# Kernel optimization log

Measured on AMD Instinct MI355X. Metric: run time of the kernel, lower is better.

The kernel has to match this reference:

```python
import jax, jax.numpy as jnp
import numpy as np

B, N, DIM = 2, 2048, 1024
HEADS, DIM_HEAD = 16, 64
INNER = HEADS * DIM_HEAD  # 1024
SCALE = DIM_HEAD ** -0.5


def setup_inputs() -> dict:
    key = jax.random.key(0)
    ks = jax.random.split(key, 8)
    s = DIM ** -0.5
    return {
        "x1": jax.random.normal(ks[0], (B, N, DIM), jnp.float32),
        "x2": jax.random.normal(ks[1], (B, N, DIM), jnp.float32),
        "W_qkv1": jax.random.normal(ks[2], (DIM, INNER * 3), jnp.float32) * s,
        "W_qkv2": jax.random.normal(ks[3], (DIM, INNER * 3), jnp.float32) * s,
        "W_out1": jax.random.normal(ks[4], (INNER, DIM), jnp.float32) * s,
        "b_out1": jnp.zeros((DIM,), jnp.float32),
        "W_out2": jax.random.normal(ks[5], (INNER, DIM), jnp.float32) * s,
        "b_out2": jnp.zeros((DIM,), jnp.float32),
    }


def _split_heads(t):
    # [b, n, (h d)] -> [b, h, n, d]
    b, n, _ = t.shape
    return t.reshape(b, n, HEADS, DIM_HEAD).transpose(0, 2, 1, 3)


def _merge_heads(t):
    # [b, h, n, d] -> [b, n, (h d)]
    b, h, n, d = t.shape
    return t.transpose(0, 2, 1, 3).reshape(b, n, h * d)


def reference(x1, x2, W_qkv1, W_qkv2, W_out1, b_out1, W_out2, b_out2):
    qkv1 = x1 @ W_qkv1  # [b, n, 3*inner]
    qkv2 = x2 @ W_qkv2
    q1, k1, v1 = [_split_heads(t) for t in jnp.split(qkv1, 3, axis=-1)]
    q2, k2, v2 = [_split_heads(t) for t in jnp.split(qkv2, 3, axis=-1)]

    # direction 1: queries from stream 2 attend to keys/values of stream 1
    dots1 = jnp.einsum('bhid,bhjd->bhij', q2, k1) * SCALE
    attn1 = jax.nn.softmax(dots1, axis=-1)
    out1 = jnp.einsum('bhij,bhjd->bhid', attn1, v1)
    out1 = _merge_heads(out1) @ W_out1 + b_out1

    # direction 2: queries from stream 1 attend to keys/values of stream 2
    dots2 = jnp.einsum('bhid,bhjd->bhij', q1, k2) * SCALE
    attn2 = jax.nn.softmax(dots2, axis=-1)
    out2 = jnp.einsum('bhij,bhjd->bhid', attn2, v2)
    out2 = _merge_heads(out2) @ W_out2 + b_out2

    return (out1, out2)
```

## Files before the change

### kernel.cpp

```cpp
#include <hip/hip_runtime.h>
#include <cmath>

typedef __attribute__((ext_vector_type(8))) short short8;
typedef __attribute__((ext_vector_type(4))) float f32x4;
typedef __attribute__((ext_vector_type(16))) float f32x16;
using u16 = unsigned short;

#define DEV static __device__ __forceinline__

DEV u16 f2bf(float f) {
  union { float f; unsigned u; } v; v.f = f;
  unsigned r = v.u + 0x7FFFu + ((v.u >> 16) & 1u);
  return (u16)(r >> 16);
}

DEV unsigned cvtpk(float lo, float hi_) {
  unsigned d;
  asm("v_cvt_pk_bf16_f32 %0, %1, %2" : "=v"(d) : "v"(lo), "v"(hi_));
  return d;
}

DEV void gld16(const void* g, void* l) {
  __builtin_amdgcn_global_load_lds(
      (const __attribute__((address_space(1))) unsigned*)g,
      (__attribute__((address_space(3))) unsigned*)l, 16, 0, 0);
}

__global__ void probe_scale(float* out) {
  if (threadIdx.x == 0 && blockIdx.x == 0) {
    float b = __builtin_amdgcn_exp2f(1.0f);
    out[0] = 0.125f / logf(b);
    out[1] = (fabsf(b - 2.0f) < 1e-3f) ? 0.0f : 1.0f;
  }
}

__global__ __launch_bounds__(256) void conv_f32_bf16(const float* __restrict__ s0,
                                                     const float* __restrict__ s1,
                                                     u16* __restrict__ d0,
                                                     u16* __restrict__ d1, int n8) {
  const float* src = blockIdx.z ? s1 : s0;
  u16* dst = blockIdx.z ? d1 : d0;
  int i = blockIdx.x * 256 + threadIdx.x;
  if (i >= n8) return;
  const float4* s = reinterpret_cast<const float4*>(src) + (size_t)i * 2;
  float4 a = s[0], b = s[1];
  union { u16 s[8]; uint4 v; } t;
  t.s[0]=f2bf(a.x); t.s[1]=f2bf(a.y); t.s[2]=f2bf(a.z); t.s[3]=f2bf(a.w);
  t.s[4]=f2bf(b.x); t.s[5]=f2bf(b.y); t.s[6]=f2bf(b.z); t.s[7]=f2bf(b.w);
  reinterpret_cast<uint4*>(dst)[i] = t.v;
}

__global__ __launch_bounds__(256) void transpose_w(const float* __restrict__ s0,
                                                   const float* __restrict__ s1,
                                                   u16* __restrict__ d0,
                                                   u16* __restrict__ d1, int R, int C,
                                                   int qcols,
                                                   const float* __restrict__ qscale_p) {
  const float* src = blockIdx.z ? s1 : s0;
  u16* dst = blockIdx.z ? d1 : d0;
  const float qscale = qscale_p ? qscale_p[0] : 1.0f;
  __shared__ float tile[32][33];
  int tx = threadIdx.x & 31, ty = threadIdx.x >> 5;
  int rb = blockIdx.y * 32, cb = blockIdx.x * 32;
#pragma unroll
  for (int j = 0; j < 32; j += 8)
    tile[ty + j][tx] = src[(size_t)(rb + ty + j) * C + cb + tx];
  __syncthreads();
#pragma unroll
  for (int j = 0; j < 32; j += 8) {
    int c = cb + ty + j;
    float sc = (c < qcols) ? qscale : 1.0f;
    dst[(size_t)c * R + rb + tx] = f2bf(tile[tx][ty + j] * sc);
  }
}

extern __shared__ char dsmem[];

__global__ __launch_bounds__(512, 2) void gemm256(
    const u16* __restrict__ A0, const u16* __restrict__ A1,
    const u16* __restrict__ B0, const u16* __restrict__ B1,
    u16* __restrict__ Q0, u16* __restrict__ Q1,
    u16* __restrict__ V0, u16* __restrict__ V1) {
  const int orig = blockIdx.x;
  const int wgid = (orig & 7) * 48 + (orig >> 3);
  const int z = wgid / 192, rr_ = wgid % 192;
  const int bx = rr_ / 12, by = rr_ % 12;
  const u16* Ag = z ? A1 : A0;
  const u16* Bg = z ? B1 : B0;
  const size_t m0 = (size_t)bx * 256, n0 = (size_t)by * 256;
  const int K = 1024;

  const int tid = threadIdx.x;
  const int lane = tid & 63;
  const int wave = tid >> 6;
  const int wm = wave >> 2, wn = wave & 3;
  const int lr = lane & 15, lk = lane >> 4;

  f32x4 acc[8][4] = {};

  auto STG = [&](int buf, int kt, int opi) {
    int idx = opi * 512 + tid;
    char* base = dsmem + buf * 65536;
    if (idx < 2048) {
      int r = idx >> 3, c = idx & 7;
      gld16(Ag + (m0 + r) * (size_t)K + kt * 64 + ((c ^ (r & 7)) * 8), base + idx * 16);
    } else {
      int j = idx - 2048;
      int r = j >> 3, c = j & 7;
      gld16(Bg + (n0 + r) * (size_t)K + kt * 64 + ((c ^ (r & 7)) * 8), base + 32768 + j * 16);
    }
  };
  auto DSA = [&](short8* af, int buf, int mg, int kh) {
#pragma unroll
    for (int i = 0; i < 4; ++i) {
      int row = wm * 128 + (mg * 4 + i) * 16 + lr;
      af[i] = *reinterpret_cast<const short8*>(
          dsmem + buf * 65536 + row * 128 + (((kh * 4 + lk) ^ (row & 7)) * 16));
    }
  };
  auto DSB = [&](short8* bf_, int buf, int kh) {
#pragma unroll
    for (int j = 0; j < 4; ++j) {
      int row = wn * 64 + j * 16 + lr;
      bf_[j] = *reinterpret_cast<const short8*>(
          dsmem + buf * 65536 + 32768 + row * 128 + (((kh * 4 + lk) ^ (row & 7)) * 16));
    }
  };

#pragma unroll
  for (int o = 0; o < 8; ++o) STG(0, 0, o);
  asm volatile("s_waitcnt vmcnt(0)" ::: "memory");
  __syncthreads();

  int cur = 0;
  for (int kt = 0; kt < 16; ++kt) {
    short8 af[4], bf_[4];
    const int more = (kt < 15);

    DSA(af, cur, 0, 0); DSB(bf_, cur, 0);
    if (more) { STG(cur ^ 1, kt + 1, 0); STG(cur ^ 1, kt + 1, 1);
                STG(cur ^ 1, kt + 1, 2); STG(cur ^ 1, kt + 1, 3); }
    __builtin_amdgcn_s_barrier();
    asm volatile("s_waitcnt lgkmcnt(0)" ::: "memory");
    __builtin_amdgcn_sched_barrier(0);
    __builtin_amdgcn_s_setprio(1);
#pragma unroll
    for (int i = 0; i < 4; ++i)
#pragma unroll
      for (int j = 0; j < 4; ++j)
        acc[i][j] = __builtin_amdgcn_mfma_f32_16x16x32_bf16(af[i], bf_[j], acc[i][j], 0, 0, 0);
    __builtin_amdgcn_s_setprio(0);
    __builtin_amdgcn_s_barrier();

    DSA(af, cur, 1, 0);
    if (more) { STG(cur ^ 1, kt + 1, 4); STG(cur ^ 1, kt + 1, 5);
                STG(cur ^ 1, kt + 1, 6); STG(cur ^ 1, kt + 1, 7); }
    __builtin_amdgcn_s_barrier();
    asm volatile("s_waitcnt lgkmcnt(0)" ::: "memory");
    __builtin_amdgcn_sched_barrier(0);
    __builtin_amdgcn_s_setprio(1);
#pragma unroll
    for (int i = 0; i < 4; ++i)
#pragma unroll
      for (int j = 0; j < 4; ++j)
        acc[4 + i][j] = __builtin_amdgcn_mfma_f32_16x16x32_bf16(af[i], bf_[j], acc[4 + i][j], 0, 0, 0);
    __builtin_amdgcn_s_setprio(0);
    __builtin_amdgcn_s_barrier();

    DSA(af, cur, 0, 1); DSB(bf_, cur, 1);
    __builtin_amdgcn_s_barrier();
    asm volatile("s_waitcnt lgkmcnt(0)" ::: "memory");
    __builtin_amdgcn_sched_barrier(0);
    __builtin_amdgcn_s_setprio(1);
#pragma unroll
    for (int i = 0; i < 4; ++i)
#pragma unroll
      for (int j = 0; j < 4; ++j)
        acc[i][j] = __builtin_amdgcn_mfma_f32_16x16x32_bf16(af[i], bf_[j], acc[i][j], 0, 0, 0);
    __builtin_amdgcn_s_setprio(0);
    __builtin_amdgcn_s_barrier();

    DSA(af, cur, 1, 1);
    __builtin_amdgcn_s_barrier();
    asm volatile("s_waitcnt lgkmcnt(0)" ::: "memory");
    __builtin_amdgcn_sched_barrier(0);
    __builtin_amdgcn_s_setprio(1);
#pragma unroll
    for (int i = 0; i < 4; ++i)
#pragma unroll
      for (int j = 0; j < 4; ++j)
        acc[4 + i][j] = __builtin_amdgcn_mfma_f32_16x16x32_bf16(af[i], bf_[j], acc[4 + i][j], 0, 0, 0);
    __builtin_amdgcn_s_setprio(0);
    asm volatile("s_waitcnt vmcnt(0)" ::: "memory");
    __builtin_amdgcn_s_barrier();
    cur ^= 1;
  }

  const int row0 = (int)m0 + wm * 128;
  const int col0 = (int)n0 + wn * 64;
  u16* Qo = z ? Q1 : Q0;
  u16* Vo = z ? V1 : V0;
  if (col0 < 2048) {
#pragma unroll
    for (int mf = 0; mf < 8; ++mf)
#pragma unroll
      for (int nf = 0; nf < 4; ++nf) {
        int col = col0 + nf * 16 + lr;
#pragma unroll
        for (int g = 0; g < 4; ++g) {
          int row = row0 + mf * 16 + lk * 4 + g;
          Qo[(size_t)row * 3072 + col] = f2bf(acc[mf][nf][g]);
        }
      }
  } else {
#pragma unroll
    for (int mf = 0; mf < 8; ++mf)
#pragma unroll
      for (int nf = 0; nf < 4; ++nf) {
        int col = col0 + nf * 16 + lr;
        int row = row0 + mf * 16 + lk * 4;
        size_t vbase = ((size_t)((row >> 11) * 1024 + (col - 2048))) * 2048 + (row & 2047);
        union { u16 s[4]; unsigned long long v; } pk;
#pragma unroll
        for (int g = 0; g < 4; ++g) pk.s[g] = f2bf(acc[mf][nf][g]);
        *reinterpret_cast<unsigned long long*>(Vo + vbase) = pk.v;
      }
  }
}

__global__ __launch_bounds__(256) void gemm_bt(
    const u16* __restrict__ A0, const u16* __restrict__ A1,
    const u16* __restrict__ B0, const u16* __restrict__ B1,
    float* __restrict__ Cf0, float* __restrict__ Cf1,
    const float* __restrict__ bias0, const float* __restrict__ bias1,
    int M, int N, int K) {
  const int z = blockIdx.z;
  const u16* A  = z ? A1 : A0;
  const u16* Bt = z ? B1 : B0;
  float* Cf = z ? Cf1 : Cf0;
  const float* bias = z ? bias1 : bias0;

  __shared__ __align__(16) char smem[32768];
  char* As = smem;
  char* Bs = smem + 16384;
  const int tid = threadIdx.x;
  const int lane = tid & 63, wave = tid >> 6;
  const int wm = wave >> 1, wn = wave & 1;
  const int lr = lane & 15, lk = lane >> 4;
  const size_t m0 = (size_t)blockIdx.x * 128, n0 = (size_t)blockIdx.y * 128;

  f32x4 acc[4][4] = {};

  for (int k0 = 0; k0 < K; k0 += 64) {
    __syncthreads();
#pragma unroll
    for (int i = 0; i < 4; ++i) {
      int idx = tid + i * 256;
      int r = idx >> 3, c = idx & 7;
      int cs = c ^ (r & 7);
      gld16(A + (m0 + r) * (size_t)K + k0 + cs * 8, As + idx * 16);
    }
#pragma unroll
    for (int i = 0; i < 4; ++i) {
      int idx = tid + i * 256;
      int r = idx >> 3, c = idx & 7;
      int cs = c ^ (r & 7);
      gld16(Bt + (n0 + r) * (size_t)K + k0 + cs * 8, Bs + idx * 16);
    }
    __syncthreads();
#pragma unroll
    for (int kk = 0; kk < 2; ++kk) {
      short8 af[4], bfr[4];
#pragma unroll
      for (int mf = 0; mf < 4; ++mf) {
        int r = wm * 64 + mf * 16 + lr;
        af[mf] = *reinterpret_cast<const short8*>(As + r * 128 + (((kk * 4 + lk) ^ (r & 7)) * 16));
      }
#pragma unroll
      for (int nf = 0; nf < 4; ++nf) {
        int r = wn * 64 + nf * 16 + lr;
        bfr[nf] = *reinterpret_cast<const short8*>(Bs + r * 128 + (((kk * 4 + lk) ^ (r & 7)) * 16));
      }
#pragma unroll
      for (int mf = 0; mf < 4; ++mf)
#pragma unroll
        for (int nf = 0; nf < 4; ++nf)
          acc[mf][nf] = __builtin_amdgcn_mfma_f32_16x16x32_bf16(af[mf], bfr[nf], acc[mf][nf], 0, 0, 0);
    }
  }
  const int row0 = (int)m0 + wm * 64, col0 = (int)n0 + wn * 64;
#pragma unroll
  for (int nf = 0; nf < 4; ++nf) {
    int col = col0 + nf * 16 + lr;
    float bv = bias[col];
#pragma unroll
    for (int mf = 0; mf < 4; ++mf)
#pragma unroll
      for (int g = 0; g < 4; ++g) {
        int row = row0 + mf * 16 + lk * 4 + g;
        Cf[(size_t)row * N + col] = acc[mf][nf][g] + bv;
      }
  }
}

#define KOFF0 0
#define VOFF0 (8192 + 64)
#define KOFF1 (16384 + 128)
#define VOFF1 (KOFF1 + 8192 + 64)

__global__ __launch_bounds__(256, 2) void flash(
    const u16* __restrict__ qkv1, const u16* __restrict__ qkv2,
    const u16* __restrict__ vT1, const u16* __restrict__ vT2,
    u16* __restrict__ ao1, u16* __restrict__ ao2,
    const float* __restrict__ sflag) {
  const int bid = blockIdx.x;
  const int bh_dir = bid & 63;
  const int qt = bid >> 6;
  const int dir = bh_dir >> 5;
  const int bh = bh_dir & 31;
  const int b = bh >> 4, h = bh & 15;
  const u16* qkvQ  = dir ? qkv1 : qkv2;
  const u16* qkvKV = dir ? qkv2 : qkv1;
  const u16* vT    = dir ? vT2 : vT1;
  u16* Oout        = dir ? ao2 : ao1;

  const bool nat = (sflag[1] != 0.0f);

  __shared__ __align__(16) char smem[33024];

  const int tid = threadIdx.x;
  const int lane = tid & 63, wave = tid >> 6;
  const int l31 = lane & 31, hi = lane >> 5;

  const int qbase = qt * 256 + wave * 64;
  const u16* qp0 = qkvQ + (size_t)(b * 2048 + qbase + l31) * 3072 + h * 64 + hi * 8;
  const u16* qp1 = qp0 + (size_t)32 * 3072;
  short8 qf0[4], qf1[4];
#pragma unroll
  for (int c = 0; c < 4; ++c) {
    qf0[c] = *reinterpret_cast<const short8*>(qp0 + c * 16);
    qf1[c] = *reinterpret_cast<const short8*>(qp1 + c * 16);
  }

  auto STAGE = [&](char* kb, char* vb, int kv0) {
#pragma unroll
    for (int i = 0; i < 2; ++i) {
      int idx = tid + i * 256;
      int r = idx >> 3, c = idx & 7, cs = c ^ (r & 7);
      gld16(qkvKV + (size_t)(b * 2048 + kv0 + r) * 3072 + 1024 + h * 64 + cs * 8, kb + idx * 16);
      gld16(vT + (size_t)(bh * 64 + r) * 2048 + kv0 + cs * 8, vb + idx * 16);
    }
  };

  auto EXPV = [&](f32x16& S) {
    if (nat) {
#pragma unroll
      for (int r = 0; r < 16; ++r) S[r] = __builtin_amdgcn_exp2f(S[r]);
    } else {
#pragma unroll
      for (int r = 0; r < 16; ++r) S[r] = __builtin_exp2f(S[r]);
    }
  };

  short8 ones;
#pragma unroll
  for (int j = 0; j < 8; ++j) ones[j] = (short)0x3F80;

  f32x16 oA0 = {}, oA1 = {}, oB0 = {}, oB1 = {}, laccA = {}, laccB = {};

  STAGE(smem + KOFF0, smem + VOFF0, 0);

  union U8 { unsigned u[4]; short8 s8; };

  for (int t = 0; t < 32; ++t) {
    char* Ks = smem + ((t & 1) ? KOFF1 : KOFF0);
    char* Vs = smem + ((t & 1) ? VOFF1 : VOFF0);
    __syncthreads();
    if (t < 31)
      STAGE(smem + ((t & 1) ? KOFF0 : KOFF1), smem + ((t & 1) ? VOFF0 : VOFF1), (t + 1) * 64);

    short8 kf[8];
#pragma unroll
    for (int c = 0; c < 4; ++c) {
      int sw = ((c * 2 + hi) ^ (l31 & 7)) * 16;
      kf[c]     = *reinterpret_cast<const short8*>(Ks + l31 * 128 + sw);
      kf[c + 4] = *reinterpret_cast<const short8*>(Ks + (32 + l31) * 128 + sw);
    }

    f32x16 sA0 = {}, sA1 = {};
#pragma unroll
    for (int c = 0; c < 4; ++c) {
      sA0 = __builtin_amdgcn_mfma_f32_32x32x16_bf16(kf[c],     qf0[c], sA0, 0, 0, 0);
      sA1 = __builtin_amdgcn_mfma_f32_32x32x16_bf16(kf[c + 4], qf0[c], sA1, 0, 0, 0);
    }
    EXPV(sA0); EXPV(sA1);
    short8 paA[4];
#pragma unroll
    for (int kc = 0; kc < 4; ++kc) {
      const f32x16& S = (kc < 2) ? sA0 : sA1;
      int rb = (kc & 1) * 8;
      unsigned a0 = cvtpk(S[rb + 0], S[rb + 1]);
      unsigned b0 = cvtpk(S[rb + 4], S[rb + 5]);
      asm volatile("v_permlane32_swap_b32 %0, %1" : "+v"(a0), "+v"(b0));
      unsigned a1 = cvtpk(S[rb + 2], S[rb + 3]);
      unsigned b1 = cvtpk(S[rb + 6], S[rb + 7]);
      asm volatile("v_permlane32_swap_b32 %0, %1" : "+v"(a1), "+v"(b1));
      U8 u; u.u[0] = a0; u.u[1] = a1; u.u[2] = b0; u.u[3] = b1;
      paA[kc] = u.s8;
    }

    f32x16 sB0 = {}, sB1 = {};
#pragma unroll
    for (int c = 0; c < 4; ++c) {
      sB0 = __builtin_amdgcn_mfma_f32_32x32x16_bf16(kf[c],     qf1[c], sB0, 0, 0, 0);
      sB1 = __builtin_amdgcn_mfma_f32_32x32x16_bf16(kf[c + 4], qf1[c], sB1, 0, 0, 0);
    }

    short8 vf[8];
#pragma unroll
    for (int kc = 0; kc < 4; ++kc) {
      int sw = ((kc * 2 + hi) ^ (l31 & 7)) * 16;
      vf[kc]     = *reinterpret_cast<const short8*>(Vs + l31 * 128 + sw);
      vf[kc + 4] = *reinterpret_cast<const short8*>(Vs + (32 + l31) * 128 + sw);
    }

    EXPV(sB0); EXPV(sB1);
    short8 paB[4];
#pragma unroll
    for (int kc = 0; kc < 4; ++kc) {
      const f32x16& S = (kc < 2) ? sB0 : sB1;
      int rb = (kc & 1) * 8;
      unsigned a0 = cvtpk(S[rb + 0], S[rb + 1]);
      unsigned b0 = cvtpk(S[rb + 4], S[rb + 5]);
      asm volatile("v_permlane32_swap_b32 %0, %1" : "+v"(a0), "+v"(b0));
      unsigned a1 = cvtpk(S[rb + 2], S[rb + 3]);
      unsigned b1 = cvtpk(S[rb + 6], S[rb + 7]);
      asm volatile("v_permlane32_swap_b32 %0, %1" : "+v"(a1), "+v"(b1));
      U8 u; u.u[0] = a0; u.u[1] = a1; u.u[2] = b0; u.u[3] = b1;
      paB[kc] = u.s8;
    }

#pragma unroll
    for (int kc = 0; kc < 4; ++kc) {
      oA0 = __builtin_amdgcn_mfma_f32_32x32x16_bf16(paA[kc], vf[kc],     oA0, 0, 0, 0);
      oA1 = __builtin_amdgcn_mfma_f32_32x32x16_bf16(paA[kc], vf[kc + 4], oA1, 0, 0, 0);
      oB0 = __builtin_amdgcn_mfma_f32_32x32x16_bf16(paB[kc], vf[kc],     oB0, 0, 0, 0);
      oB1 = __builtin_amdgcn_mfma_f32_32x32x16_bf16(paB[kc], vf[kc + 4], oB1, 0, 0, 0);
      laccA = __builtin_amdgcn_mfma_f32_32x32x16_bf16(paA[kc], ones, laccA, 0, 0, 0);
      laccB = __builtin_amdgcn_mfma_f32_32x32x16_bf16(paB[kc], ones, laccB, 0, 0, 0);
    }
  }

  const int rowbase = b * 2048 + qt * 256 + wave * 64;
#pragma unroll
  for (int r = 0; r < 16; ++r) {
    int q = (r & 3) + 8 * (r >> 2) + 4 * hi;
    float liA = 1.0f / laccA[r], liB = 1.0f / laccB[r];
    u16* opA = Oout + (size_t)(rowbase + q) * 1024 + h * 64 + l31;
    u16* opB = opA + (size_t)32 * 1024;
    opA[0]  = f2bf(oA0[r] * liA);
    opA[32] = f2bf(oA1[r] * liA);
    opB[0]  = f2bf(oB0[r] * liB);
    opB[32] = f2bf(oB1[r] * liB);
  }
}

extern "C" void kernel_launch(void* const* d_in, const int* in_sizes, int n_in,
                              void* d_out, int out_size, void* d_ws, size_t ws_size,
                              hipStream_t stream) {
  const float* x1  = (const float*)d_in[0];
  const float* x2  = (const float*)d_in[1];
  const float* Wq1 = (const float*)d_in[2];
  const float* Wq2 = (const float*)d_in[3];
  const float* Wo1 = (const float*)d_in[4];
  const float* bo1 = (const float*)d_in[5];
  const float* Wo2 = (const float*)d_in[6];
  const float* bo2 = (const float*)d_in[7];
  float* out = (float*)d_out;

  char* ws = (char*)d_ws;
  u16* x1b  = (u16*)(ws + 0);
  u16* x2b  = (u16*)(ws + 8388608);
  u16* Wq1t = (u16*)(ws + 16777216);
  u16* Wq2t = (u16*)(ws + 23068672);
  u16* Wo1t = (u16*)(ws + 29360128);
  u16* Wo2t = (u16*)(ws + 31457280);
  u16* qkv1 = (u16*)(ws + 33554432);
  u16* qkv2 = (u16*)(ws + 58720256);
  u16* vT1  = (u16*)(ws + 83886080);
  u16* vT2  = (u16*)(ws + 92274688);
  u16* ao1  = (u16*)(ws + 100663296);
  u16* ao2  = (u16*)(ws + 109051904);

  float* scale_buf = (float*)(qkv1 + 2048);

  hipFuncSetAttribute(reinterpret_cast<const void*>(gemm256),
                      hipFuncAttributeMaxDynamicSharedMemorySize, 131072);

  probe_scale<<<dim3(1), 64, 0, stream>>>(scale_buf);

  conv_f32_bf16<<<dim3(2048, 1, 2), 256, 0, stream>>>(x1, x2, x1b, x2b, 4194304 / 8);
  transpose_w<<<dim3(96, 32, 2), 256, 0, stream>>>(Wq1, Wq2, Wq1t, Wq2t, 1024, 3072,
                                                   1024, scale_buf);
  transpose_w<<<dim3(32, 32, 2), 256, 0, stream>>>(Wo1, Wo2, Wo1t, Wo2t, 1024, 1024,
                                                   0, nullptr);

  gemm256<<<dim3(384), 512, 131072, stream>>>(x1b, x2b, Wq1t, Wq2t,
                                              qkv1, qkv2, vT1, vT2);

  flash<<<dim3(512), 256, 0, stream>>>(qkv1, qkv2, vT1, vT2, ao1, ao2, scale_buf);

  gemm_bt<<<dim3(32, 8, 2), 256, 0, stream>>>(ao1, ao2, Wo1t, Wo2t,
                                              out, out + 4194304, bo1, bo2,
                                              4096, 1024, 1024);
}
```

Before: 214.5 us.

## Pipeline output GEMM, merge weight transposes, fold exp probe into conversion

Replaces the output-projection GEMM with a 512-thread, 256x128-tile kernel. It double-buffers global-to-LDS loads, splits each K-step into two MFMA phases with barriers and priority bumps, and remaps block IDs to group tiles. The exp-scale probe kernel is folded into the input conversion kernel, and the two weight-transpose launches become one four-slice launch, cutting launch count. The flash kernel's native exp path uses batched inline v_exp_f32 asm. The gains depend on removing launch overhead and overlapping loads with MFMA in the last GEMM. The price is more LDS per block, which may lower occupancy, and fragile hand-placed waitcnt and barrier sequences.

Result: faster. 197.4 us (-8.0%).

```diff
diff --git a/kernel.cpp b/kernel.cpp
--- a/kernel.cpp
+++ b/kernel.cpp
@@ -26,42 +26,66 @@
       (__attribute__((address_space(3))) unsigned*)l, 16, 0, 0);
 }
 
-__global__ void probe_scale(float* out) {
-  if (threadIdx.x == 0 && blockIdx.x == 0) {
-    float b = __builtin_amdgcn_exp2f(1.0f);
-    out[0] = 0.125f / logf(b);
-    out[1] = (fabsf(b - 2.0f) < 1e-3f) ? 0.0f : 1.0f;
-  }
+DEV float hw_exp(float x) {
+  float y;
+  asm volatile("v_exp_f32 %0, %1\n\ts_nop 1" : "=v"(y) : "v"(x));
+  return y;
 }
 
 __global__ __launch_bounds__(256) void conv_f32_bf16(const float* __restrict__ s0,
                                                      const float* __restrict__ s1,
                                                      u16* __restrict__ d0,
-                                                     u16* __restrict__ d1, int n8) {
+                                                     u16* __restrict__ d1, int n8,
+                                                     float* __restrict__ scale_out) {
   const float* src = blockIdx.z ? s1 : s0;
   u16* dst = blockIdx.z ? d1 : d0;
   int i = blockIdx.x * 256 + threadIdx.x;
-  if (i >= n8) return;
-  const float4* s = reinterpret_cast<const float4*>(src) + (size_t)i * 2;
-  float4 a = s[0], b = s[1];
-  union { u16 s[8]; uint4 v; } t;
-  t.s[0]=f2bf(a.x); t.s[1]=f2bf(a.y); t.s[2]=f2bf(a.z); t.s[3]=f2bf(a.w);
-  t.s[4]=f2bf(b.x); t.s[5]=f2bf(b.y); t.s[6]=f2bf(b.z); t.s[7]=f2bf(b.w);
-  reinterpret_cast<uint4*>(dst)[i] = t.v;
-}
-
-__global__ __launch_bounds__(256) void transpose_w(const float* __restrict__ s0,
-                                                   const float* __restrict__ s1,
-                                                   u16* __restrict__ d0,
-                                                   u16* __restrict__ d1, int R, int C,
-                                                   int qcols,
-                                                   const float* __restrict__ qscale_p) {
-  const float* src = blockIdx.z ? s1 : s0;
-  u16* dst = blockIdx.z ? d1 : d0;
-  const float qscale = qscale_p ? qscale_p[0] : 1.0f;
+  if (i < n8) {
+    const float4* s = reinterpret_cast<const float4*>(src) + (size_t)i * 2;
+    float4 a = s[0], b = s[1];
+    union { u16 s[8]; uint4 v; } t;
+    t.s[0]=f2bf(a.x); t.s[1]=f2bf(a.y); t.s[2]=f2bf(a.z); t.s[3]=f2bf(a.w);
+    t.s[4]=f2bf(b.x); t.s[5]=f2bf(b.y); t.s[6]=f2bf(b.z); t.s[7]=f2bf(b.w);
+    reinterpret_cast<uint4*>(dst)[i] = t.v;
+  }
+  if (blockIdx.x == 0 && blockIdx.z == 0 && threadIdx.x == 0) {
+    float one;
+    asm volatile("v_mov_b32 %0, 1.0" : "=v"(one));
+    float bb = hw_exp(one);
+    float lnb = logf(bb);
+    bool ok = (fabsf(bb - 2.0f) < 0.25f) && (lnb > 0.1f);
+    const float xs[3] = {0.3333f, -5.7f, 9.1f};
+    for (int k = 0; k < 3; ++k) {
+      float xo;
+      asm volatile("v_mov_b32 %0, %1" : "=v"(xo) : "v"(xs[k]));
+      float yn = hw_exp(xo);
+      float yr = expf(lnb * xs[k]);
+      ok = ok && (fabsf(yn - yr) <= 2e-4f * fabsf(yr));
+    }
+    scale_out[0] = ok ? (0.125f / lnb) : (0.125f / 0.69314718056f);
+    scale_out[1] = ok ? 1.0f : 0.0f;
+  }
+}
+
+__global__ __launch_bounds__(256) void transpose_w(
+    const float* __restrict__ q1, const float* __restrict__ q2,
+    const float* __restrict__ o1, const float* __restrict__ o2,
+    u16* __restrict__ q1t, u16* __restrict__ q2t,
+    u16* __restrict__ o1t, u16* __restrict__ o2t,
+    const float* __restrict__ scale) {
+  const int z = blockIdx.z;
+  const float* src; u16* dst; int C, qcols;
+  if (z == 0)      { src = q1; dst = q1t; C = 3072; qcols = 1024; }
+  else if (z == 1) { src = q2; dst = q2t; C = 3072; qcols = 1024; }
+  else if (z == 2) { src = o1; dst = o1t; C = 1024; qcols = 0; }
+  else             { src = o2; dst = o2t; C = 1024; qcols = 0; }
+  const int R = 1024;
+  int cb = blockIdx.x * 32;
+  if (cb >= C) return;
+  const float qscale = scale[0];
   __shared__ float tile[32][33];
   int tx = threadIdx.x & 31, ty = threadIdx.x >> 5;
-  int rb = blockIdx.y * 32, cb = blockIdx.x * 32;
+  int rb = blockIdx.y * 32;
 #pragma unroll
   for (int j = 0; j < 32; j += 8)
     tile[ty + j][tx] = src[(size_t)(rb + ty + j) * C + cb + tx];
@@ -228,67 +252,102 @@
   }
 }
 
-__global__ __launch_bounds__(256) void gemm_bt(
+__global__ __launch_bounds__(512, 2) void gemm_op(
     const u16* __restrict__ A0, const u16* __restrict__ A1,
     const u16* __restrict__ B0, const u16* __restrict__ B1,
-    float* __restrict__ Cf0, float* __restrict__ Cf1,
-    const float* __restrict__ bias0, const float* __restrict__ bias1,
-    int M, int N, int K) {
-  const int z = blockIdx.z;
-  const u16* A  = z ? A1 : A0;
-  const u16* Bt = z ? B1 : B0;
-  float* Cf = z ? Cf1 : Cf0;
-  const float* bias = z ? bias1 : bias0;
-
-  __shared__ __align__(16) char smem[32768];
-  char* As = smem;
-  char* Bs = smem + 16384;
+    float* __restrict__ C0, float* __restrict__ C1,
+    const float* __restrict__ b0_, const float* __restrict__ b1_) {
+  const int orig = blockIdx.x;
+  const int wgid = (orig & 7) * 32 + (orig >> 3);
+  const int z = wgid / 128, rr_ = wgid % 128;
+  const int bx = rr_ / 8, by = rr_ % 8;
+  const u16* Ag = z ? A1 : A0;
+  const u16* Bg = z ? B1 : B0;
+  float* Cf = z ? C1 : C0;
+  const float* bias = z ? b1_ : b0_;
+  const size_t m0 = (size_t)bx * 256, n0 = (size_t)by * 128;
+  const int K = 1024;
+
   const int tid = threadIdx.x;
-  const int lane = tid & 63, wave = tid >> 6;
+  const int lane = tid & 63;
+  const int wave = tid >> 6;
   const int wm = wave >> 1, wn = wave & 1;
   const int lr = lane & 15, lk = lane >> 4;
-  const size_t m0 = (size_t)blockIdx.x * 128, n0 = (size_t)blockIdx.y * 128;
 
   f32x4 acc[4][4] = {};
 
-  for (int k0 = 0; k0 < K; k0 += 64) {
-    __syncthreads();
+  auto STG = [&](int buf, int kt, int opi) {
+    int idx = opi * 512 + tid;
+    char* base = dsmem + buf * 49152;
+    if (idx < 2048) {
+      int r = idx >> 3, c = idx & 7;
+      gld16(Ag + (m0 + r) * (size_t)K + kt * 64 + ((c ^ (r & 7)) * 8), base + idx * 16);
+    } else {
+      int j = idx - 2048;
+      int r = j >> 3, c = j & 7;
+      gld16(Bg + (n0 + r) * (size_t)K + kt * 64 + ((c ^ (r & 7)) * 8), base + 32768 + j * 16);
+    }
+  };
+  auto DSA = [&](short8* af, int buf, int kh) {
 #pragma unroll
     for (int i = 0; i < 4; ++i) {
-      int idx = tid + i * 256;
-      int r = idx >> 3, c = idx & 7;
-      int cs = c ^ (r & 7);
-      gld16(A + (m0 + r) * (size_t)K + k0 + cs * 8, As + idx * 16);
-    }
-#pragma unroll
-    for (int i = 0; i < 4; ++i) {
-      int idx = tid + i * 256;
-      int r = idx >> 3, c = idx & 7;
-      int cs = c ^ (r & 7);
-      gld16(Bt + (n0 + r) * (size_t)K + k0 + cs * 8, Bs + idx * 16);
-    }
-    __syncthreads();
-#pragma unroll
-    for (int kk = 0; kk < 2; ++kk) {
-      short8 af[4], bfr[4];
-#pragma unroll
-      for (int mf = 0; mf < 4; ++mf) {
-        int r = wm * 64 + mf * 16 + lr;
-        af[mf] = *reinterpret_cast<const short8*>(As + r * 128 + (((kk * 4 + lk) ^ (r & 7)) * 16));
-      }
-#pragma unroll
-      for (int nf = 0; nf < 4; ++nf) {
-        int r = wn * 64 + nf * 16 + lr;
-        bfr[nf] = *reinterpret_cast<const short8*>(Bs + r * 128 + (((kk * 4 + lk) ^ (r & 7)) * 16));
-      }
-#pragma unroll
-      for (int mf = 0; mf < 4; ++mf)
-#pragma unroll
-        for (int nf = 0; nf < 4; ++nf)
-          acc[mf][nf] = __builtin_amdgcn_mfma_f32_16x16x32_bf16(af[mf], bfr[nf], acc[mf][nf], 0, 0, 0);
-    }
-  }
-  const int row0 = (int)m0 + wm * 64, col0 = (int)n0 + wn * 64;
+      int row = wm * 64 + i * 16 + lr;
+      af[i] = *reinterpret_cast<const short8*>(
+          dsmem + buf * 49152 + row * 128 + (((kh * 4 + lk) ^ (row & 7)) * 16));
+    }
+  };
+  auto DSB = [&](short8* bf_, int buf, int kh) {
+#pragma unroll
+    for (int j = 0; j < 4; ++j) {
+      int row = wn * 64 + j * 16 + lr;
+      bf_[j] = *reinterpret_cast<const short8*>(
+          dsmem + buf * 49152 + 32768 + row * 128 + (((kh * 4 + lk) ^ (row & 7)) * 16));
+    }
+  };
+
+#pragma unroll
+  for (int o = 0; o < 6; ++o) STG(0, 0, o);
+  asm volatile("s_waitcnt vmcnt(0)" ::: "memory");
+  __syncthreads();
+
+  int cur = 0;
+  for (int kt = 0; kt < 16; ++kt) {
+    short8 af[4], bf_[4];
+    const int more = (kt < 15);
+
+    DSA(af, cur, 0); DSB(bf_, cur, 0);
+    if (more) { STG(cur ^ 1, kt + 1, 0); STG(cur ^ 1, kt + 1, 1); STG(cur ^ 1, kt + 1, 2);
+                STG(cur ^ 1, kt + 1, 3); STG(cur ^ 1, kt + 1, 4); STG(cur ^ 1, kt + 1, 5); }
+    __builtin_amdgcn_s_barrier();
+    asm volatile("s_waitcnt lgkmcnt(0)" ::: "memory");
+    __builtin_amdgcn_sched_barrier(0);
+    __builtin_amdgcn_s_setprio(1);
+#pragma unroll
+    for (int i = 0; i < 4; ++i)
+#pragma unroll
+      for (int j = 0; j < 4; ++j)
+        acc[i][j] = __builtin_amdgcn_mfma_f32_16x16x32_bf16(af[i], bf_[j], acc[i][j], 0, 0, 0);
+    __builtin_amdgcn_s_setprio(0);
+    __builtin_amdgcn_s_barrier();
+
+    DSA(af, cur, 1); DSB(bf_, cur, 1);
+    __builtin_amdgcn_s_barrier();
+    asm volatile("s_waitcnt lgkmcnt(0)" ::: "memory");
+    __builtin_amdgcn_sched_barrier(0);
+    __builtin_amdgcn_s_setprio(1);
+#pragma unroll
+    for (int i = 0; i < 4; ++i)
+#pragma unroll
+      for (int j = 0; j < 4; ++j)
+        acc[i][j] = __builtin_amdgcn_mfma_f32_16x16x32_bf16(af[i], bf_[j], acc[i][j], 0, 0, 0);
+    __builtin_amdgcn_s_setprio(0);
+    asm volatile("s_waitcnt vmcnt(0)" ::: "memory");
+    __builtin_amdgcn_s_barrier();
+    cur ^= 1;
+  }
+
+  const int row0 = (int)m0 + wm * 64;
+  const int col0 = (int)n0 + wn * 64;
 #pragma unroll
   for (int nf = 0; nf < 4; ++nf) {
     int col = col0 + nf * 16 + lr;
@@ -298,7 +357,7 @@
 #pragma unroll
       for (int g = 0; g < 4; ++g) {
         int row = row0 + mf * 16 + lk * 4 + g;
-        Cf[(size_t)row * N + col] = acc[mf][nf][g] + bv;
+        Cf[(size_t)row * 1024 + col] = acc[mf][nf][g] + bv;
       }
   }
 }
@@ -355,7 +414,13 @@
   auto EXPV = [&](f32x16& S) {
     if (nat) {
 #pragma unroll
-      for (int r = 0; r < 16; ++r) S[r] = __builtin_amdgcn_exp2f(S[r]);
+      for (int r = 0; r < 16; r += 4) {
+        float a = S[r], bq = S[r + 1], c = S[r + 2], d = S[r + 3];
+        asm volatile("v_exp_f32 %0, %0\n\tv_exp_f32 %1, %1\n\t"
+                     "v_exp_f32 %2, %2\n\tv_exp_f32 %3, %3\n\ts_nop 1"
+                     : "+v"(a), "+v"(bq), "+v"(c), "+v"(d));
+        S[r] = a; S[r + 1] = bq; S[r + 2] = c; S[r + 3] = d;
+      }
     } else {
 #pragma unroll
       for (int r = 0; r < 16; ++r) S[r] = __builtin_exp2f(S[r]);
@@ -496,21 +561,19 @@
 
   hipFuncSetAttribute(reinterpret_cast<const void*>(gemm256),
                       hipFuncAttributeMaxDynamicSharedMemorySize, 131072);
-
-  probe_scale<<<dim3(1), 64, 0, stream>>>(scale_buf);
-
-  conv_f32_bf16<<<dim3(2048, 1, 2), 256, 0, stream>>>(x1, x2, x1b, x2b, 4194304 / 8);
-  transpose_w<<<dim3(96, 32, 2), 256, 0, stream>>>(Wq1, Wq2, Wq1t, Wq2t, 1024, 3072,
-                                                   1024, scale_buf);
-  transpose_w<<<dim3(32, 32, 2), 256, 0, stream>>>(Wo1, Wo2, Wo1t, Wo2t, 1024, 1024,
-                                                   0, nullptr);
+  hipFuncSetAttribute(reinterpret_cast<const void*>(gemm_op),
+                      hipFuncAttributeMaxDynamicSharedMemorySize, 98304);
+
+  conv_f32_bf16<<<dim3(2048, 1, 2), 256, 0, stream>>>(x1, x2, x1b, x2b, 4194304 / 8,
+                                                      scale_buf);
+  transpose_w<<<dim3(96, 32, 4), 256, 0, stream>>>(Wq1, Wq2, Wo1, Wo2,
+                                                   Wq1t, Wq2t, Wo1t, Wo2t, scale_buf);
 
   gemm256<<<dim3(384), 512, 131072, stream>>>(x1b, x2b, Wq1t, Wq2t,
                                               qkv1, qkv2, vT1, vT2);
 
   flash<<<dim3(512), 256, 0, stream>>>(qkv1, qkv2, vT1, vT2, ao1, ao2, scale_buf);
 
-  gemm_bt<<<dim3(32, 8, 2), 256, 0, stream>>>(ao1, ao2, Wo1t, Wo2t,
-                                              out, out + 4194304, bo1, bo2,
-                                              4096, 1024, 1024);
-}
+  gemm_op<<<dim3(256), 512, 98304, stream>>>(ao1, ao2, Wo1t, Wo2t,
+                                             out, out + 4194304, bo1, bo2);
+}
```
